# Kernel tuning notes

Measured on AMD Instinct MI355X. Metric: run time of the kernel, lower is better.

## Reference

```python
import jax, jax.numpy as jnp
import numpy as np

N = 8192
HIDDEN = 1024
PROJ = 128
T = 0.07
LN_EPS = 1e-12


def _neg_indices(n):
    # Static [n, n-2] index matrix: for row i, all j except j==i and the
    # paired sample j == (i + n//2) % n. Computed with numpy (n is static).
    half = n // 2
    idx = np.arange(n)
    mask = np.ones((n, n), dtype=bool)
    mask[idx, idx] = False
    mask[idx, (idx + half) % n] = False
    return np.nonzero(mask)[1].reshape(n, n - 2)


def setup_inputs() -> dict:
    key = jax.random.key(0)
    ks = jax.random.split(key, 3)
    scale = 1.0 / np.sqrt(HIDDEN)
    return {
        "x": jax.random.normal(ks[0], (N, HIDDEN), dtype=jnp.float32),
        "dense_w": jax.random.normal(ks[1], (HIDDEN, HIDDEN), dtype=jnp.float32) * scale,
        "dense_b": jnp.zeros((HIDDEN,), dtype=jnp.float32),
        "ln_gamma": jnp.ones((HIDDEN,), dtype=jnp.float32),
        "ln_beta": jnp.zeros((HIDDEN,), dtype=jnp.float32),
        "dec_w": jax.random.normal(ks[2], (HIDDEN, PROJ), dtype=jnp.float32) * scale,
        "dec_b": jnp.zeros((PROJ,), dtype=jnp.float32),
    }


def reference(x, dense_w, dense_b, ln_gamma, ln_beta, dec_w, dec_b):
    # dense -> gelu (exact, erf-based as in BERT) -> layernorm -> decoder
    h = x @ dense_w + dense_b
    h = jax.nn.gelu(h, approximate=False)
    mu = jnp.mean(h, axis=-1, keepdims=True)
    var = jnp.mean(jnp.square(h - mu), axis=-1, keepdims=True)
    h = (h - mu) * jax.lax.rsqrt(var + LN_EPS) * ln_gamma + ln_beta
    z = h @ dec_w + dec_b  # [N, 128]

    n = z.shape[0]
    half = n // 2
    # positive logit: dot(z_i, z_partner)
    l_pos = jnp.sum(z[:half] * z[half:], axis=-1)  # [N/2]
    l_pos = jnp.concatenate([l_pos, l_pos])[:, None]  # [N, 1]

    # full similarity matrix, then gather the N-2 negatives per row
    sims = z @ z.T  # [N, N]
    neg_idx = jnp.asarray(_neg_indices(n))  # static [N, N-2]
    l_neg = jnp.take_along_axis(sims, neg_idx, axis=1)  # [N, N-2]

    logits = jnp.concatenate([l_pos, l_neg], axis=1) / T  # [N, N-1]
    # CrossEntropyLoss with labels == 0
    loss = jnp.mean(jax.nn.logsumexp(logits, axis=-1) - logits[:, 0])
    return loss
```

## Files before the change

kernel.cpp:

```cpp
#include <hip/hip_runtime.h>
#include <math.h>
#include <stdint.h>

#define NN 8192
#define HID 1024
#define PROJ 128

constexpr float INV_T = 1.0f / 0.07f;
constexpr float LN_EPS = 1e-12f;
constexpr float CC = 14.285714285714286f * 1.4426950408889634f;

typedef __bf16 bf16x8 __attribute__((ext_vector_type(8)));
typedef float f32x4 __attribute__((ext_vector_type(4)));

#define EXP2(x) __builtin_amdgcn_exp2f(x)

#define GLD16(g, l)                                                     \
  __builtin_amdgcn_global_load_lds(                                     \
      (const __attribute__((address_space(1))) uint32_t*)(g),           \
      (__attribute__((address_space(3))) uint32_t*)(l), 16, 0, 0)

__device__ __forceinline__ uint16_t f2bf(float f) {
  union { float f; uint32_t u; } c; c.f = f;
  uint32_t r = (c.u + 0x7FFFu + ((c.u >> 16) & 1u)) >> 16;
  return (uint16_t)r;
}
__device__ __forceinline__ float bf2f(uint16_t u) {
  union { uint32_t u; float f; } c; c.u = ((uint32_t)u) << 16;
  return c.f;
}

__device__ __forceinline__ float gelu_f(float v) {
  float w = v * v;
  float u = v * fmaf(w, 0.0356774081f, 0.7978845608f);
  float e = EXP2(u * -2.8853900818f);
  return v * __builtin_amdgcn_rcpf(1.0f + e);
}

__global__ __launch_bounds__(256) void k_conv(const float* __restrict__ in,
                                              uint16_t* __restrict__ out,
                                              float* __restrict__ sums,
                                              float* __restrict__ c_e) {
  const int b = blockIdx.x, t = threadIdx.x;
  if (b < 64) sums[b * 256 + t] = 0.f;
  else if (b == 64) c_e[t] = 0.f;
  int i = (b * 256 + t) * 4;
  float4 v = *(const float4*)(in + i);
  ushort4 o;
  o.x = f2bf(v.x); o.y = f2bf(v.y); o.z = f2bf(v.z); o.w = f2bf(v.w);
  *(ushort4*)(out + i) = o;
}

__global__ __launch_bounds__(256) void k_t1(const float* __restrict__ in,
                                            uint16_t* __restrict__ out,
                                            int R, int C) {
  __shared__ uint16_t t[32][33];
  const int cb = blockIdx.x * 32, rb = blockIdx.y * 32;
  const int tr = threadIdx.x >> 3, tc4 = (threadIdx.x & 7) * 4;
  float4 v = *(const float4*)(in + (size_t)(rb + tr) * C + cb + tc4);
  t[tc4 + 0][tr] = f2bf(v.x);
  t[tc4 + 1][tr] = f2bf(v.y);
  t[tc4 + 2][tr] = f2bf(v.z);
  t[tc4 + 3][tr] = f2bf(v.w);
  __syncthreads();
  const int oc = threadIdx.x >> 3, or4 = (threadIdx.x & 7) * 4;
  ushort4 o;
  o.x = t[oc][or4 + 0]; o.y = t[oc][or4 + 1];
  o.z = t[oc][or4 + 2]; o.w = t[oc][or4 + 3];
  *(ushort4*)(out + (size_t)(cb + oc) * R + rb + or4) = o;
}

__global__ __launch_bounds__(256) void k_t2(const float* __restrict__ in,
                                            const float* __restrict__ gamma,
                                            const float* __restrict__ beta,
                                            uint16_t* __restrict__ out,
                                            float* __restrict__ c_e) {
  __shared__ float tg[32][33];
  __shared__ float tb[32][33];
  const int cb = blockIdx.x * 32, rb = blockIdx.y * 32;
  const int tr = threadIdx.x >> 3, tc4 = (threadIdx.x & 7) * 4;
  const float g = gamma[rb + tr], be = beta[rb + tr];
  float4 v = *(const float4*)(in + (size_t)(rb + tr) * PROJ + cb + tc4);
  tg[tc4 + 0][tr] = g * v.x;  tb[tc4 + 0][tr] = be * v.x;
  tg[tc4 + 1][tr] = g * v.y;  tb[tc4 + 1][tr] = be * v.y;
  tg[tc4 + 2][tr] = g * v.z;  tb[tc4 + 2][tr] = be * v.z;
  tg[tc4 + 3][tr] = g * v.w;  tb[tc4 + 3][tr] = be * v.w;
  __syncthreads();
  const int oc = threadIdx.x >> 3, or4 = (threadIdx.x & 7) * 4;
  ushort4 o;
  o.x = f2bf(tg[oc][or4 + 0]); o.y = f2bf(tg[oc][or4 + 1]);
  o.z = f2bf(tg[oc][or4 + 2]); o.w = f2bf(tg[oc][or4 + 3]);
  *(ushort4*)(out + (size_t)(cb + oc) * HID + rb + or4) = o;
  if (threadIdx.x < 32) {
    float sc = 0.f, se = 0.f;
#pragma unroll
    for (int d = 0; d < 32; ++d) { sc += tg[threadIdx.x][d]; se += tb[threadIdx.x][d]; }
    atomicAdd(c_e + cb + threadIdx.x, sc);
    atomicAdd(c_e + 128 + cb + threadIdx.x, se);
  }
}

__global__ __launch_bounds__(256) void k_gemm1(
    const uint16_t* __restrict__ Ab, const uint16_t* __restrict__ Bt,
    const float* __restrict__ bias, uint16_t* __restrict__ Hout,
    float* __restrict__ sums) {
  __shared__ __align__(16) uint16_t As[2 * 64 * 32];
  __shared__ __align__(16) uint16_t Bs[2 * 128 * 32];
  const int tid = threadIdx.x;
  const int bn = blockIdx.x * 128, bm = blockIdx.y * 64;
  const int wave = tid >> 6, lane = tid & 63;
  const int wx = wave & 1, wy = wave >> 1;
  const int col = lane & 15, quad = lane >> 4;
  f32x4 acc[2][4] = {};
  const char* Abase = (const char*)Ab;
  const char* Bbase = (const char*)Bt;
  for (int k0 = 0; k0 < HID; k0 += 64) {
    __syncthreads();
#pragma unroll
    for (int l = 0; l < 2; ++l) {
      int off = tid * 16 + l * 4096;
      int h = off >> 12, row = (off >> 6) & 63, inner = off & 63;
      GLD16(Abase + ((size_t)(bm + row) * HID + k0 + h * 32) * 2 + inner,
            (char*)As + off);
    }
#pragma unroll
    for (int l = 0; l < 4; ++l) {
      int off = tid * 16 + l * 4096;
      int h = off >> 13, row = (off >> 6) & 127, inner = off & 63;
      GLD16(Bbase + ((size_t)(bn + row) * HID + k0 + h * 32) * 2 + inner,
            (char*)Bs + off);
    }
    __syncthreads();
#pragma unroll
    for (int h = 0; h < 2; ++h) {
      bf16x8 a[2], b[4];
#pragma unroll
      for (int mt = 0; mt < 2; ++mt)
        a[mt] = *(const bf16x8*)&As[h * 2048 +
                                    (wy * 32 + mt * 16 + col) * 32 + quad * 8];
#pragma unroll
      for (int nt = 0; nt < 4; ++nt)
        b[nt] = *(const bf16x8*)&Bs[h * 4096 +
                                    (wx * 64 + nt * 16 + col) * 32 + quad * 8];
#pragma unroll
      for (int mt = 0; mt < 2; ++mt)
#pragma unroll
        for (int nt = 0; nt < 4; ++nt)
          acc[mt][nt] = __builtin_amdgcn_mfma_f32_16x16x32_bf16(
              a[mt], b[nt], acc[mt][nt], 0, 0, 0);
    }
  }
  float rsum[2][4] = {}, rsq[2][4] = {};
#pragma unroll
  for (int nt = 0; nt < 4; ++nt) {
    int gj = bn + wx * 64 + nt * 16 + col;
    float bv = bias[gj];
#pragma unroll
    for (int mt = 0; mt < 2; ++mt)
#pragma unroll
      for (int r = 0; r < 4; ++r) {
        int gi = bm + wy * 32 + mt * 16 + quad * 4 + r;
        float gl = gelu_f(acc[mt][nt][r] + bv);
        Hout[(size_t)gi * HID + gj] = f2bf(gl);
        rsum[mt][r] += gl;
        rsq[mt][r] = fmaf(gl, gl, rsq[mt][r]);
      }
  }
#pragma unroll
  for (int mt = 0; mt < 2; ++mt)
#pragma unroll
    for (int r = 0; r < 4; ++r) {
      float s1 = rsum[mt][r], s2 = rsq[mt][r];
#pragma unroll
      for (int off = 1; off < 16; off <<= 1) {
        s1 += __shfl_xor(s1, off, 64);
        s2 += __shfl_xor(s2, off, 64);
      }
      if (col == 0) {
        int gi = bm + wy * 32 + mt * 16 + quad * 4 + r;
        atomicAdd(&sums[gi], s1);
        atomicAdd(&sums[NN + gi], s2);
      }
    }
}

__global__ __launch_bounds__(256) void k_gemm2(
    const uint16_t* __restrict__ Hb, const uint16_t* __restrict__ Wt2,
    const float* __restrict__ bd, const float* __restrict__ sums,
    const float* __restrict__ c_e, uint16_t* __restrict__ Z) {
  __shared__ __align__(16) uint16_t As2[32 * 32];
  __shared__ __align__(16) uint16_t Bs2[128 * 32];
  __shared__ float muS[32], rS[32];
  const int tid = threadIdx.x;
  const int bm = blockIdx.x * 32;
  const int wave = tid >> 6, lane = tid & 63;
  const int wx = wave & 1, wy = wave >> 1;
  const int col = lane & 15, quad = lane >> 4;
  if (tid < 32) {
    float s = sums[bm + tid], q = sums[NN + bm + tid];
    float mu = s * (1.0f / HID);
    float var = q * (1.0f / HID) - mu * mu;
    muS[tid] = mu;
    rS[tid] = rsqrtf(var + LN_EPS);
  }
  f32x4 acc[4] = {};
  const char* Abase = (const char*)Hb;
  const char* Bbase = (const char*)Wt2;
  for (int k0 = 0; k0 < HID; k0 += 32) {
    __syncthreads();
    if (tid < 128) {
      int off = tid * 16;
      int row = off >> 6, inner = off & 63;
      GLD16(Abase + ((size_t)(bm + row) * HID + k0) * 2 + inner,
            (char*)As2 + off);
    }
#pragma unroll
    for (int l = 0; l < 2; ++l) {
      int off = tid * 16 + l * 4096;
      int row = off >> 6, inner = off & 63;
      GLD16(Bbase + ((size_t)row * HID + k0) * 2 + inner, (char*)Bs2 + off);
    }
    __syncthreads();
    bf16x8 a = *(const bf16x8*)&As2[(wy * 16 + col) * 32 + quad * 8];
#pragma unroll
    for (int nt = 0; nt < 4; ++nt) {
      bf16x8 b = *(const bf16x8*)&Bs2[(wx * 64 + nt * 16 + col) * 32 + quad * 8];
      acc[nt] = __builtin_amdgcn_mfma_f32_16x16x32_bf16(a, b, acc[nt], 0, 0, 0);
    }
  }
#pragma unroll
  for (int nt = 0; nt < 4; ++nt) {
    int gj = wx * 64 + nt * 16 + col;
    float ck = c_e[gj], ek = c_e[128 + gj] + bd[gj];
#pragma unroll
    for (int r = 0; r < 4; ++r) {
      int li = wy * 16 + quad * 4 + r;
      float mu = muS[li], rr = rS[li];
      float z = fmaf(rr, acc[nt][r], fmaf(-rr * mu, ck, ek));
      Z[(size_t)(bm + li) * PROJ + gj] = f2bf(z);
    }
  }
}

__device__ __forceinline__ void lse4(float& m, float& s, float v0, float v1,
                                     float v2, float v3) {
  float lm = fmaxf(fmaxf(v0, v1), fmaxf(v2, v3));
  float mn = fmaxf(m, lm);
  float tn = mn * CC;
  float rs = EXP2(fmaf(m, CC, -tn));
  float e = EXP2(fmaf(v0, CC, -tn)) + EXP2(fmaf(v1, CC, -tn)) +
            EXP2(fmaf(v2, CC, -tn)) + EXP2(fmaf(v3, CC, -tn));
  s = fmaf(s, rs, e);
  m = mn;
}

__global__ __launch_bounds__(256) void k_sim(const uint16_t* __restrict__ Z,
                                             float* __restrict__ m_part,
                                             float* __restrict__ s_part,
                                             float* __restrict__ pos_arr) {
  const int tid = threadIdx.x;
  const int wave = tid >> 6, lane = tid & 63;
  const int col = lane & 15, quad = lane >> 4;
  const int wrow0 = blockIdx.x * 128 + wave * 32;
  const int chunk = blockIdx.y;
  bf16x8 afr[2][4];
#pragma unroll
  for (int mt = 0; mt < 2; ++mt)
#pragma unroll
    for (int kc = 0; kc < 4; ++kc)
      afr[mt][kc] = *(const bf16x8*)(Z +
          (size_t)(wrow0 + mt * 16 + col) * PROJ + kc * 32 + quad * 8);
  float ms[8], ss[8];
#pragma unroll
  for (int i = 0; i < 8; ++i) { ms[i] = -INFINITY; ss[i] = 0.f; }
  const int diag_t = wrow0 & ~63;
  const int pos_t = ((wrow0 + NN / 2) & (NN - 1)) & ~63;
  const int jbase = chunk * 512;
  for (int t8 = 0; t8 < 8; ++t8) {
    const int jt = jbase + t8 * 64;
    f32x4 acc[2][4] = {};
#pragma unroll
    for (int kc = 0; kc < 4; ++kc) {
      bf16x8 b[4];
#pragma unroll
      for (int nt = 0; nt < 4; ++nt)
        b[nt] = *(const bf16x8*)(Z + (size_t)(jt + nt * 16 + col) * PROJ +
                                 kc * 32 + quad * 8);
#pragma unroll
      for (int mt = 0; mt < 2; ++mt)
#pragma unroll
        for (int nt = 0; nt < 4; ++nt)
          acc[mt][nt] = __builtin_amdgcn_mfma_f32_16x16x32_bf16(
              afr[mt][kc], b[nt], acc[mt][nt], 0, 0, 0);
    }
    if (jt != diag_t && jt != pos_t) {
#pragma unroll
      for (int mt = 0; mt < 2; ++mt)
#pragma unroll
        for (int r = 0; r < 4; ++r)
          lse4(ms[mt * 4 + r], ss[mt * 4 + r], acc[mt][0][r], acc[mt][1][r],
               acc[mt][2][r], acc[mt][3][r]);
    } else {
      const bool isd = (jt == diag_t);
#pragma unroll
      for (int mt = 0; mt < 2; ++mt)
#pragma unroll
        for (int r = 0; r < 4; ++r) {
          int gi = wrow0 + mt * 16 + quad * 4 + r;
          int partner = (gi + NN / 2) & (NN - 1);
          float v[4];
#pragma unroll
          for (int nt = 0; nt < 4; ++nt) {
            int gj = jt + nt * 16 + col;
            float d = acc[mt][nt][r];
            if (!isd && gj == partner) pos_arr[gi] = d;
            v[nt] = (isd && gj == gi) ? -INFINITY : d;
          }
          lse4(ms[mt * 4 + r], ss[mt * 4 + r], v[0], v[1], v[2], v[3]);
        }
    }
  }
#pragma unroll
  for (int ri = 0; ri < 8; ++ri) {
#pragma unroll
    for (int off = 1; off < 16; off <<= 1) {
      float om = __shfl_xor(ms[ri], off, 64);
      float os = __shfl_xor(ss[ri], off, 64);
      float mn = fmaxf(ms[ri], om);
      float tn = mn * CC;
      ss[ri] = fmaf(ss[ri], EXP2(fmaf(ms[ri], CC, -tn)),
                    os * EXP2(fmaf(om, CC, -tn)));
      ms[ri] = mn;
    }
  }
  if (col == 0) {
#pragma unroll
    for (int ri = 0; ri < 8; ++ri) {
      int gi = wrow0 + (ri >> 2) * 16 + quad * 4 + (ri & 3);
      m_part[(size_t)chunk * NN + gi] = ms[ri];
      s_part[(size_t)chunk * NN + gi] = ss[ri];
    }
  }
}

__global__ __launch_bounds__(256) void k_combine(
    const float* __restrict__ m_part, const float* __restrict__ s_part,
    const float* __restrict__ pos_arr, float* __restrict__ row_loss) {
  const int i = blockIdx.x * 256 + threadIdx.x;
  float M = -INFINITY;
#pragma unroll
  for (int p = 0; p < 16; ++p) M = fmaxf(M, m_part[(size_t)p * NN + i]);
  float S = 0.f;
  float t = M * CC;
#pragma unroll
  for (int p = 0; p < 16; ++p)
    S += s_part[(size_t)p * NN + i] * EXP2(fmaf(m_part[(size_t)p * NN + i], CC, -t));
  row_loss[i] = (M - pos_arr[i]) * INV_T + logf(S);
}

__global__ __launch_bounds__(256) void k_final(
    const float* __restrict__ row_loss, float* __restrict__ out) {
  const int tid = threadIdx.x;
  float s = 0.f;
#pragma unroll
  for (int l = 0; l < 32; ++l) s += row_loss[tid + l * 256];
#pragma unroll
  for (int off = 32; off > 0; off >>= 1) s += __shfl_down(s, off);
  __shared__ float red[4];
  const int wave = tid >> 6, lane = tid & 63;
  if (lane == 0) red[wave] = s;
  __syncthreads();
  if (tid == 0) out[0] = (red[0] + red[1] + red[2] + red[3]) * (1.0f / NN);
}

extern "C" void kernel_launch(void* const* d_in, const int* in_sizes, int n_in,
                              void* d_out, int out_size, void* d_ws,
                              size_t ws_size, hipStream_t stream) {
  const float* x       = (const float*)d_in[0];
  const float* dense_w = (const float*)d_in[1];
  const float* dense_b = (const float*)d_in[2];
  const float* ln_g    = (const float*)d_in[3];
  const float* ln_b    = (const float*)d_in[4];
  const float* dec_w   = (const float*)d_in[5];
  const float* dec_b   = (const float*)d_in[6];
  float* out = (float*)d_out;
  char* ws = (char*)d_ws;
  uint16_t* xb      = (uint16_t*)(ws);
  uint16_t* wt      = (uint16_t*)(ws + 16777216);
  uint16_t* h       = (uint16_t*)(ws + 18874368);
  uint16_t* z       = (uint16_t*)(ws);
  float*    m_part  = (float*)(ws + 16777216);
  float*    s_part  = (float*)(ws + 17301504);
  uint16_t* wt2     = (uint16_t*)(ws + 35651584);
  float*    sums    = (float*)(ws + 35913728);
  float*    c_e     = (float*)(ws + 35979264);
  float*    pos_arr = (float*)(ws + 35980288);
  float*    row_loss= (float*)(ws + 36013056);

  k_conv<<<dim3(NN * HID / 1024), 256, 0, stream>>>(x, xb, sums, c_e);
  k_t1<<<dim3(32, 32), 256, 0, stream>>>(dense_w, wt, HID, HID);
  k_t2<<<dim3(PROJ / 32, HID / 32), 256, 0, stream>>>(dec_w, ln_g, ln_b, wt2,
                                                      c_e);
  k_gemm1<<<dim3(8, 128), 256, 0, stream>>>(xb, wt, dense_b, h, sums);
  k_gemm2<<<dim3(NN / 32), 256, 0, stream>>>(h, wt2, dec_b, sums, c_e, z);
  k_sim<<<dim3(64, 16), 256, 0, stream>>>(z, m_part, s_part, pos_arr);
  k_combine<<<dim3(NN / 256), 256, 0, stream>>>(m_part, s_part, pos_arr,
                                                row_loss);
  k_final<<<dim3(1), 256, 0, stream>>>(row_loss, out);
}
```

Before: 213.8 us.

## Stage similarity B tiles through swizzled double-buffered LDS and widen row tiles

The similarity kernel now loads each 64-column tile of Z into shared memory once per block, using async global-to-LDS copies with an XOR swizzle and double buffering. Each wave's B fragments are then read from LDS instead of every wave reading them separately from global memory. Each wave also covers 64 rows instead of 32, which doubles the MFMA work per B load and halves the block count. The cost is more registers for accumulators and A fragments (launch bounds ask for two blocks per CU), plus a barrier on every tile.

```diff
diff --git a/kernel.cpp b/kernel.cpp
--- a/kernel.cpp
+++ b/kernel.cpp
@@ -254,40 +254,64 @@
   m = mn;
 }
 
-__global__ __launch_bounds__(256) void k_sim(const uint16_t* __restrict__ Z,
-                                             float* __restrict__ m_part,
-                                             float* __restrict__ s_part,
-                                             float* __restrict__ pos_arr) {
+__global__ __launch_bounds__(256, 2) void k_sim(const uint16_t* __restrict__ Z,
+                                                float* __restrict__ m_part,
+                                                float* __restrict__ s_part,
+                                                float* __restrict__ pos_arr) {
+  __shared__ __align__(16) uint16_t Bsh[2][64 * 128];
   const int tid = threadIdx.x;
   const int wave = tid >> 6, lane = tid & 63;
   const int col = lane & 15, quad = lane >> 4;
-  const int wrow0 = blockIdx.x * 128 + wave * 32;
+  const int wrow0 = blockIdx.x * 256 + wave * 64;
   const int chunk = blockIdx.y;
-  bf16x8 afr[2][4];
-#pragma unroll
-  for (int mt = 0; mt < 2; ++mt)
+  const char* Zb = (const char*)Z;
+
+  bf16x8 afr[4][4];
+#pragma unroll
+  for (int mt = 0; mt < 4; ++mt)
 #pragma unroll
     for (int kc = 0; kc < 4; ++kc)
       afr[mt][kc] = *(const bf16x8*)(Z +
           (size_t)(wrow0 + mt * 16 + col) * PROJ + kc * 32 + quad * 8);
-  float ms[8], ss[8];
-#pragma unroll
-  for (int i = 0; i < 8; ++i) { ms[i] = -INFINITY; ss[i] = 0.f; }
-  const int diag_t = wrow0 & ~63;
-  const int pos_t = ((wrow0 + NN / 2) & (NN - 1)) & ~63;
+
+  float ms[16], ss[16];
+#pragma unroll
+  for (int i = 0; i < 16; ++i) { ms[i] = -INFINITY; ss[i] = 0.f; }
+
+  const int diag_t = wrow0;
+  const int pos_t = (wrow0 + NN / 2) & (NN - 1);
   const int jbase = chunk * 512;
-  for (int t8 = 0; t8 < 8; ++t8) {
-    const int jt = jbase + t8 * 64;
-    f32x4 acc[2][4] = {};
+
+#define STAGE(t, bufv)                                                      \
+  {                                                                         \
+    const int j0s = jbase + (t) * 64;                                       \
+    _Pragma("unroll") for (int l = 0; l < 4; ++l) {                         \
+      int off = tid * 16 + l * 4096;                                        \
+      int row = off >> 8;                                                   \
+      int p = (off >> 4) & 15;                                              \
+      GLD16(Zb + (size_t)(j0s + row) * 256 + ((p ^ (row & 7)) << 4),        \
+            (char*)&Bsh[bufv][0] + off);                                    \
+    }                                                                       \
+  }
+
+  STAGE(0, 0);
+  for (int t = 0; t < 8; ++t) {
+    const int buf = t & 1;
+    __syncthreads();
+    if (t < 7) STAGE(t + 1, buf ^ 1);
+    const int jt = jbase + t * 64;
+    f32x4 acc[4][4] = {};
 #pragma unroll
     for (int kc = 0; kc < 4; ++kc) {
       bf16x8 b[4];
 #pragma unroll
-      for (int nt = 0; nt < 4; ++nt)
-        b[nt] = *(const bf16x8*)(Z + (size_t)(jt + nt * 16 + col) * PROJ +
-                                 kc * 32 + quad * 8);
-#pragma unroll
-      for (int mt = 0; mt < 2; ++mt)
+      for (int nt = 0; nt < 4; ++nt) {
+        int r = nt * 16 + col;
+        b[nt] = *(const bf16x8*)&Bsh[buf][r * 128 +
+                                         (((kc * 4 + quad) ^ (col & 7)) << 3)];
+      }
+#pragma unroll
+      for (int mt = 0; mt < 4; ++mt)
 #pragma unroll
         for (int nt = 0; nt < 4; ++nt)
           acc[mt][nt] = __builtin_amdgcn_mfma_f32_16x16x32_bf16(
@@ -295,7 +319,7 @@
     }
     if (jt != diag_t && jt != pos_t) {
 #pragma unroll
-      for (int mt = 0; mt < 2; ++mt)
+      for (int mt = 0; mt < 4; ++mt)
 #pragma unroll
         for (int r = 0; r < 4; ++r)
           lse4(ms[mt * 4 + r], ss[mt * 4 + r], acc[mt][0][r], acc[mt][1][r],
@@ -303,7 +327,7 @@
     } else {
       const bool isd = (jt == diag_t);
 #pragma unroll
-      for (int mt = 0; mt < 2; ++mt)
+      for (int mt = 0; mt < 4; ++mt)
 #pragma unroll
         for (int r = 0; r < 4; ++r) {
           int gi = wrow0 + mt * 16 + quad * 4 + r;
@@ -320,8 +344,9 @@
         }
     }
   }
-#pragma unroll
-  for (int ri = 0; ri < 8; ++ri) {
+#undef STAGE
+#pragma unroll
+  for (int ri = 0; ri < 16; ++ri) {
 #pragma unroll
     for (int off = 1; off < 16; off <<= 1) {
       float om = __shfl_xor(ms[ri], off, 64);
@@ -335,7 +360,7 @@
   }
   if (col == 0) {
 #pragma unroll
-    for (int ri = 0; ri < 8; ++ri) {
+    for (int ri = 0; ri < 16; ++ri) {
       int gi = wrow0 + (ri >> 2) * 16 + quad * 4 + (ri & 3);
       m_part[(size_t)chunk * NN + gi] = ms[ri];
       s_part[(size_t)chunk * NN + gi] = ss[ri];
@@ -403,7 +428,7 @@
                                                       c_e);
   k_gemm1<<<dim3(8, 128), 256, 0, stream>>>(xb, wt, dense_b, h, sums);
   k_gemm2<<<dim3(NN / 32), 256, 0, stream>>>(h, wt2, dec_b, sums, c_e, z);
-  k_sim<<<dim3(64, 16), 256, 0, stream>>>(z, m_part, s_part, pos_arr);
+  k_sim<<<dim3(NN / 256, 16), 256, 0, stream>>>(z, m_part, s_part, pos_arr);
   k_combine<<<dim3(NN / 256), 256, 0, stream>>>(m_part, s_part, pos_arr,
                                                 row_loss);
   k_final<<<dim3(1), 256, 0, stream>>>(row_loss, out);
```

Measured after the change: 200.6 us. 1.07x faster.
